# Kernel optimization log

Hardware: AMD Instinct MI355X
Metric: run time of the kernel (lower is better)

## Reference

```python
import jax, jax.numpy as jnp
import numpy as np
import math

N = 30000; N0 = 18000; N1 = 12000; R = 5; E = 600000
H = 128; HM = 128; C = 8
L1 = 20.0; L2 = 30.0
THRESH = 0.3; THRESH_C = 1e-3
T_INNER = 20; K_OUTER = 8
EPS = 1e-5


def setup_inputs() -> dict:
    key = jax.random.key(0)
    ks = jax.random.split(key, 16)
    def w(k, shape):  # kaiming-ish fan_in init
        return jax.random.normal(k, shape, jnp.float32) / np.sqrt(shape[0])
    return {
        "feat0": jax.random.normal(ks[0], (N0, 256), jnp.float32),
        "feat1": jax.random.normal(ks[1], (N1, 128), jnp.float32),
        "W0": w(ks[2], (256, H)), "b0": jnp.zeros((H,), jnp.float32),
        "W1": w(ks[3], (128, H)), "b1": jnp.zeros((H,), jnp.float32),
        "Wm1": w(ks[4], (H, HM)), "bm1": jnp.zeros((HM,), jnp.float32),
        "Wm2": w(ks[5], (HM, HM)), "bm2": jnp.zeros((HM,), jnp.float32),
        "Wout": w(ks[6], (HM, C)), "bout": jnp.zeros((C,), jnp.float32),
        "src": jax.random.randint(ks[7], (E,), 0, N, jnp.int32),
        "dst": jax.random.randint(ks[8], (E,), 0, N, jnp.int32),
        "rel": jax.random.randint(ks[9], (E,), 0, R, jnp.int32),
    }


def _layernorm(z):
    m = z.mean(-1, keepdims=True)
    v = z.var(-1, keepdims=True)
    return (z - m) / jnp.sqrt(v + EPS)


def _forward(feat0, feat1, W0, b0, W1, b1, Wm1, bm1, Wm2, bm2, Wout, bout, src, dst, rel):
    # transfer (transf_type==2): per-type linear -> concat -> 2-layer MLP w/ layernorm
    h = jnp.concatenate([feat0 @ W0 + b0, feat1 @ W1 + b1], axis=0)   # (N, H)
    z = jax.nn.relu(_layernorm(h @ Wm1 + bm1))
    h = z @ Wm2 + bm2                                                 # (N, HM)
    # per-node standardization (torch std is unbiased, ddof=1), nan -> 0
    mu = h.mean(1, keepdims=True)
    sd = h.std(1, ddof=1, keepdims=True)
    out0 = jnp.nan_to_num((h - mu) / sd)

    # per-relation row degrees of the vertically stacked adjacency (R*N, N)
    key_e = rel * N + src                                             # (E,)
    deg = jax.ops.segment_sum(jnp.ones(E, jnp.float32), key_e, num_segments=R * N)
    safe = jnp.maximum(deg, 1.0)
    vals = jnp.where(deg > 0, 1.0 / safe, 0.0)[key_e]                 # row-normalized A weights
    dinv = jnp.where(deg > 0, 1.0 / jnp.sqrt(safe), 0.0)              # D^{-1/2}
    edge_dinv = dinv[key_e] * dinv[rel * N + dst]                     # (E,)
    active = (deg > 0).astype(jnp.float32).reshape(R, N)              # (R, N)

    def tv(x):  # relational total variation tr(X^T L_r X)/N, L_r = I - D^-1/2 A_r D^-1/2
        node_term = active @ (x * x).sum(1)                           # (R,)
        edot = (x[src] * x[dst]).sum(1)                               # (E,)
        edge_term = jax.ops.segment_sum(edge_dinv * edot, rel, num_segments=R)
        return (node_term - edge_term) / N

    ratio = 2.0 * L2 / L1
    c_l1tr = jnp.abs(tv(out0)).sum()
    u0 = jnp.full((R,), 1.0 / R, jnp.float32)

    def mirror_descent(u, w, l1tr):
        fi = l1tr + ratio
        def step(carry, t):
            u, act = carry
            T_t = jnp.sqrt(2.0 * math.log(R) / (t * fi * fi))
            u_ta = u * jnp.exp(-T_t * (ratio * u + w))
            u_new = u_ta / u_ta.sum()
            diff = jnp.sqrt(((u - u_new) ** 2).sum())
            u = jnp.where(act, u_new, u)
            return (u, act & (diff >= THRESH_C)), None
        ts = jnp.arange(1, T_INNER + 1, dtype=jnp.float32)
        (u, _), _ = jax.lax.scan(step, (u, jnp.array(True)), ts)
        return u

    def outer(carry, _):
        x, u, act = carry
        w = tv(x)
        l1tr = jnp.abs(w).sum()
        u = jnp.where(act, mirror_descent(u, w, l1tr), u)
        still = act & (l1tr / c_l1tr >= THRESH)
        ew = u[rel] * vals                                            # (E,)
        msg = jax.ops.segment_sum(ew[:, None] * x[dst], src, num_segments=N)  # (N, HM)
        x = jnp.where(still, x / (1.0 + L1) + (L1 / (1.0 + L1)) * msg, x)
        return (x, u, still), None

    (x, u, _), _ = jax.lax.scan(outer, (out0, u0, jnp.array(True)), None, length=K_OUTER)
    logits = x @ Wout + bout
    return logits, x, u


def reference(feat0, feat1, W0, b0, W1, b1, Wm1, bm1, Wm2, bm2, Wout, bout, src, dst, rel):
    return _forward(feat0, feat1, W0, b0, W1, b1, Wm1, bm1, Wm2, bm2, Wout, bout, src, dst, rel)
```

## Files before the change

### kernel.cpp

```cpp
#include <hip/hip_runtime.h>
#include <hip/hip_fp16.h>
#include <cmath>

typedef unsigned short ushort_t;
typedef unsigned int uint_t;

#define N_TOT 30000
#define N0_   18000
#define R_    5
#define E_    600000
#define RN    (R_ * N_TOT)
#define NC_   (N_TOT * 8)
#define NX_   (N_TOT * 128)
#define NL_   (N_TOT * 64)
#define SCAN_NB ((RN + 1023) / 1024)

typedef __attribute__((ext_vector_type(8))) short bf16x8;
typedef __attribute__((ext_vector_type(4))) float f32x4;

__device__ __forceinline__ ushort_t f2bf(float f) {
    uint_t u = __float_as_uint(f);
    uint_t r = (u + 0x7fffu + ((u >> 16) & 1u)) >> 16;
    return (ushort_t)r;
}
__device__ __forceinline__ float bflo(uint_t v) { return __uint_as_float(v << 16); }
__device__ __forceinline__ float bfhi(uint_t v) { return __uint_as_float(v & 0xffff0000u); }

__global__ void init_kernel(float* ug, int* act) {
    if (threadIdx.x < 5) ug[threadIdx.x] = 0.2f;
    if (threadIdx.x == 0) act[0] = 1;
}

__global__ __launch_bounds__(256) void cvtfeat_kernel(const float* __restrict__ in,
                                                      ushort_t* __restrict__ out,
                                                      int nelem)
{
    int i = (blockIdx.x * 256 + threadIdx.x) * 4;
    if (i >= nelem) return;
    const float4 v = *(const float4*)(in + i);
    ushort_t o0 = f2bf(v.x), o1 = f2bf(v.y), o2 = f2bf(v.z), o3 = f2bf(v.w);
    uint_t p0 = (uint_t)o0 | ((uint_t)o1 << 16);
    uint_t p1 = (uint_t)o2 | ((uint_t)o3 << 16);
    uint2* op = (uint2*)(out + i);
    *op = make_uint2(p0, p1);
}

__global__ __launch_bounds__(256) void cvtw_kernel(const float* __restrict__ W,
                                                   ushort_t* __restrict__ wt, int K)
{
    int idx = blockIdx.x * 256 + threadIdx.x;
    if (idx >= 128 * K) return;
    int j = idx / K, k = idx - j * K;
    wt[idx] = f2bf(W[k * 128 + j]);
}

__global__ __launch_bounds__(256) void mlp_mfma_kernel(
    const ushort_t* __restrict__ fb0, const ushort_t* __restrict__ fb1,
    const ushort_t* __restrict__ wt0, const ushort_t* __restrict__ wt1,
    const ushort_t* __restrict__ wtm1, const ushort_t* __restrict__ wtm2,
    const float* __restrict__ b0, const float* __restrict__ b1,
    const float* __restrict__ bm1, const float* __restrict__ bm2,
    float* __restrict__ xout, ushort_t* __restrict__ xh)
{
    const int t = threadIdx.x;
    const int lane = t & 63;
    const int wv = t >> 6;
    const int lr = lane & 15;
    const int lg = lane >> 4;
    const int row0 = blockIdx.x * 32;

    __shared__ ushort_t hls[32][136];
    __shared__ float    tls[32][132];
    __shared__ ushort_t zls[32][136];

    #pragma unroll
    for (int mt = 0; mt < 2; ++mt) {
        const int rb = row0 + mt * 16;
        const bool is0 = (rb < N0_);
        const int r = min(rb + lr, N_TOT - 1);
        const ushort_t* __restrict__ fa =
            is0 ? fb0 + (size_t)r * 256 : fb1 + (size_t)(r - N0_) * 128;
        const ushort_t* __restrict__ wt = is0 ? wt0 : wt1;
        const int K = is0 ? 256 : 128;
        const int c0 = wv * 32 + lr;

        f32x4 a0 = {0.f, 0.f, 0.f, 0.f};
        f32x4 a1 = {0.f, 0.f, 0.f, 0.f};
        for (int ks = 0; ks < K; ks += 32) {
            const bf16x8 af = *(const bf16x8*)(fa + ks + lg * 8);
            const bf16x8 wb0 = *(const bf16x8*)(wt + (size_t)c0 * K + ks + lg * 8);
            const bf16x8 wb1 = *(const bf16x8*)(wt + (size_t)(c0 + 16) * K + ks + lg * 8);
            a0 = __builtin_amdgcn_mfma_f32_16x16x32_bf16(af, wb0, a0, 0, 0, 0);
            a1 = __builtin_amdgcn_mfma_f32_16x16x32_bf16(af, wb1, a1, 0, 0, 0);
        }
        const float bb0 = is0 ? b0[c0] : b1[c0];
        const float bb1 = is0 ? b0[c0 + 16] : b1[c0 + 16];
        #pragma unroll
        for (int j = 0; j < 4; ++j) {
            hls[mt * 16 + lg * 4 + j][c0]      = f2bf(a0[j] + bb0);
            hls[mt * 16 + lg * 4 + j][c0 + 16] = f2bf(a1[j] + bb1);
        }
    }
    __syncthreads();

    {
        const int c0 = wv * 32 + lr;
        f32x4 g00 = {0.f,0.f,0.f,0.f}, g01 = {0.f,0.f,0.f,0.f};
        f32x4 g10 = {0.f,0.f,0.f,0.f}, g11 = {0.f,0.f,0.f,0.f};
        for (int ks = 0; ks < 128; ks += 32) {
            const bf16x8 wb0 = *(const bf16x8*)(wtm1 + (size_t)c0 * 128 + ks + lg * 8);
            const bf16x8 wb1 = *(const bf16x8*)(wtm1 + (size_t)(c0 + 16) * 128 + ks + lg * 8);
            const bf16x8 af0 = *(const bf16x8*)(&hls[lr][ks + lg * 8]);
            const bf16x8 af1 = *(const bf16x8*)(&hls[16 + lr][ks + lg * 8]);
            g00 = __builtin_amdgcn_mfma_f32_16x16x32_bf16(af0, wb0, g00, 0, 0, 0);
            g01 = __builtin_amdgcn_mfma_f32_16x16x32_bf16(af0, wb1, g01, 0, 0, 0);
            g10 = __builtin_amdgcn_mfma_f32_16x16x32_bf16(af1, wb0, g10, 0, 0, 0);
            g11 = __builtin_amdgcn_mfma_f32_16x16x32_bf16(af1, wb1, g11, 0, 0, 0);
        }
        const float bb0 = bm1[c0], bb1 = bm1[c0 + 16];
        #pragma unroll
        for (int j = 0; j < 4; ++j) {
            tls[lg * 4 + j][c0]           = g00[j] + bb0;
            tls[lg * 4 + j][c0 + 16]      = g01[j] + bb1;
            tls[16 + lg * 4 + j][c0]      = g10[j] + bb0;
            tls[16 + lg * 4 + j][c0 + 16] = g11[j] + bb1;
        }
    }
    __syncthreads();

    {
        const int row = t >> 3, seg = t & 7;
        f32x4 v[4];
        float s = 0.f;
        #pragma unroll
        for (int i = 0; i < 4; ++i) {
            v[i] = *(const f32x4*)(&tls[row][seg * 16 + i * 4]);
            s += v[i][0] + v[i][1] + v[i][2] + v[i][3];
        }
        #pragma unroll
        for (int o = 1; o < 8; o <<= 1) s += __shfl_xor(s, o, 64);
        const float mean = s * (1.0f / 128.0f);
        float q = 0.f;
        #pragma unroll
        for (int i = 0; i < 4; ++i) {
            #pragma unroll
            for (int e = 0; e < 4; ++e) { float d = v[i][e] - mean; q = fmaf(d, d, q); }
        }
        #pragma unroll
        for (int o = 1; o < 8; o <<= 1) q += __shfl_xor(q, o, 64);
        const float inv = 1.0f / sqrtf(q * (1.0f / 128.0f) + 1e-5f);
        uint_t* zp = (uint_t*)&zls[row][0];
        #pragma unroll
        for (int i = 0; i < 4; ++i) {
            ushort_t z0 = f2bf(fmaxf((v[i][0] - mean) * inv, 0.0f));
            ushort_t z1 = f2bf(fmaxf((v[i][1] - mean) * inv, 0.0f));
            ushort_t z2 = f2bf(fmaxf((v[i][2] - mean) * inv, 0.0f));
            ushort_t z3 = f2bf(fmaxf((v[i][3] - mean) * inv, 0.0f));
            zp[(seg * 16 + i * 4) / 2]     = (uint_t)z0 | ((uint_t)z1 << 16);
            zp[(seg * 16 + i * 4) / 2 + 1] = (uint_t)z2 | ((uint_t)z3 << 16);
        }
    }
    __syncthreads();

    {
        const int c0 = wv * 32 + lr;
        f32x4 g00 = {0.f,0.f,0.f,0.f}, g01 = {0.f,0.f,0.f,0.f};
        f32x4 g10 = {0.f,0.f,0.f,0.f}, g11 = {0.f,0.f,0.f,0.f};
        for (int ks = 0; ks < 128; ks += 32) {
            const bf16x8 wb0 = *(const bf16x8*)(wtm2 + (size_t)c0 * 128 + ks + lg * 8);
            const bf16x8 wb1 = *(const bf16x8*)(wtm2 + (size_t)(c0 + 16) * 128 + ks + lg * 8);
            const bf16x8 af0 = *(const bf16x8*)(&zls[lr][ks + lg * 8]);
            const bf16x8 af1 = *(const bf16x8*)(&zls[16 + lr][ks + lg * 8]);
            g00 = __builtin_amdgcn_mfma_f32_16x16x32_bf16(af0, wb0, g00, 0, 0, 0);
            g01 = __builtin_amdgcn_mfma_f32_16x16x32_bf16(af0, wb1, g01, 0, 0, 0);
            g10 = __builtin_amdgcn_mfma_f32_16x16x32_bf16(af1, wb0, g10, 0, 0, 0);
            g11 = __builtin_amdgcn_mfma_f32_16x16x32_bf16(af1, wb1, g11, 0, 0, 0);
        }
        __syncthreads();
        const float bb0 = bm2[c0], bb1 = bm2[c0 + 16];
        #pragma unroll
        for (int j = 0; j < 4; ++j) {
            tls[lg * 4 + j][c0]           = g00[j] + bb0;
            tls[lg * 4 + j][c0 + 16]      = g01[j] + bb1;
            tls[16 + lg * 4 + j][c0]      = g10[j] + bb0;
            tls[16 + lg * 4 + j][c0 + 16] = g11[j] + bb1;
        }
    }
    __syncthreads();

    {
        const int row = t >> 3, seg = t & 7;
        const int n = row0 + row;
        f32x4 v[4];
        float s = 0.f;
        #pragma unroll
        for (int i = 0; i < 4; ++i) {
            v[i] = *(const f32x4*)(&tls[row][seg * 16 + i * 4]);
            s += v[i][0] + v[i][1] + v[i][2] + v[i][3];
        }
        #pragma unroll
        for (int o = 1; o < 8; o <<= 1) s += __shfl_xor(s, o, 64);
        const float mu = s * (1.0f / 128.0f);
        float q = 0.f;
        #pragma unroll
        for (int i = 0; i < 4; ++i) {
            #pragma unroll
            for (int e = 0; e < 4; ++e) { float d = v[i][e] - mu; q = fmaf(d, d, q); }
        }
        #pragma unroll
        for (int o = 1; o < 8; o <<= 1) q += __shfl_xor(q, o, 64);
        const float sd = sqrtf(q * (1.0f / 127.0f));
        const float inv = 1.0f / sd;
        if (n < N_TOT) {
            uint_t* xhp = (uint_t*)xh + (size_t)n * 64 + seg * 8;
            float* xop = xout + (size_t)n * 128 + seg * 16;
            #pragma unroll
            for (int i = 0; i < 4; ++i) {
                float rr[4];
                #pragma unroll
                for (int e = 0; e < 4; ++e) {
                    float r = (v[i][e] - mu) * inv;
                    if (!(fabsf(r) <= 3.402823466e38f)) {
                        r = (r != r) ? 0.0f : ((r > 0.0f) ? 3.402823466e38f : -3.402823466e38f);
                    }
                    rr[e] = r;
                }
                *(float4*)(xop + i * 4) = make_float4(rr[0], rr[1], rr[2], rr[3]);
                xhp[i * 2]     = (uint_t)f2bf(rr[0]) | ((uint_t)f2bf(rr[1]) << 16);
                xhp[i * 2 + 1] = (uint_t)f2bf(rr[2]) | ((uint_t)f2bf(rr[3]) << 16);
            }
        }
    }
}

__global__ void deg_kernel(const int* __restrict__ src, const int* __restrict__ rel,
                           int* __restrict__ deg_i)
{
    int e = blockIdx.x * 256 + threadIdx.x;
    if (e >= E_) return;
    atomicAdd(&deg_i[src[e] * R_ + rel[e]], 1);
}

__global__ void dinv_kernel(const int* __restrict__ deg_i, float* __restrict__ dinv)
{
    int i = blockIdx.x * 256 + threadIdx.x;
    if (i >= RN) return;
    int dg = deg_i[i];
    dinv[i] = (dg > 0) ? 1.0f / sqrtf((float)dg) : 0.0f;
}

__global__ __launch_bounds__(256) void scan1_kernel(const int* __restrict__ cnt,
                                                    int* __restrict__ rp,
                                                    int* __restrict__ bsum)
{
    __shared__ int wsum[4];
    const int t = threadIdx.x, lane = t & 63, w = t >> 6;
    const int i0 = blockIdx.x * 1024 + t * 4;
    const int v0 = (i0 + 0 < RN) ? cnt[i0 + 0] : 0;
    const int v1 = (i0 + 1 < RN) ? cnt[i0 + 1] : 0;
    const int v2 = (i0 + 2 < RN) ? cnt[i0 + 2] : 0;
    const int v3 = (i0 + 3 < RN) ? cnt[i0 + 3] : 0;
    const int s = v0 + v1 + v2 + v3;
    int sc = s;
    #pragma unroll
    for (int o = 1; o < 64; o <<= 1) { int tmp = __shfl_up(sc, o, 64); if (lane >= o) sc += tmp; }
    if (lane == 63) wsum[w] = sc;
    __syncthreads();
    int woff = 0;
    #pragma unroll
    for (int i = 0; i < 3; ++i) if (i < w) woff += wsum[i];
    int run = woff + sc - s;
    if (i0 + 0 < RN) rp[i0 + 0] = run; run += v0;
    if (i0 + 1 < RN) rp[i0 + 1] = run; run += v1;
    if (i0 + 2 < RN) rp[i0 + 2] = run; run += v2;
    if (i0 + 3 < RN) rp[i0 + 3] = run;
    if (t == 255) bsum[blockIdx.x] = woff + sc;
}

__global__ __launch_bounds__(256) void scan2_kernel(const int* __restrict__ bsum,
                                                    int* __restrict__ boff,
                                                    int* __restrict__ rp)
{
    __shared__ int wsum[4];
    const int t = threadIdx.x, lane = t & 63, w = t >> 6;
    const int v = (t < SCAN_NB) ? bsum[t] : 0;
    int sc = v;
    #pragma unroll
    for (int o = 1; o < 64; o <<= 1) { int tmp = __shfl_up(sc, o, 64); if (lane >= o) sc += tmp; }
    if (lane == 63) wsum[w] = sc;
    __syncthreads();
    int woff = 0;
    #pragma unroll
    for (int i = 0; i < 3; ++i) if (i < w) woff += wsum[i];
    boff[t] = woff + sc - v;
    if (t == 0) rp[RN] = E_;
}

__global__ __launch_bounds__(256) void scan3_kernel(int* __restrict__ rp,
                                                    const int* __restrict__ boff)
{
    const int off = boff[blockIdx.x];
    if (off == 0) return;
    const int i0 = blockIdx.x * 1024 + threadIdx.x * 4;
    if (i0 + 3 < RN) {
        int4* p = (int4*)(rp + i0);
        int4 q = *p;
        q.x += off; q.y += off; q.z += off; q.w += off;
        *p = q;
    } else {
        for (int i = 0; i < 4; ++i)
            if (i0 + i < RN) rp[i0 + i] += off;
    }
}

__global__ void scatter_kernel(const int* __restrict__ src, const int* __restrict__ dst,
                               const int* __restrict__ rel, const int* __restrict__ rp,
                               int* __restrict__ fill, const int* __restrict__ deg_i,
                               const float* __restrict__ dinv,
                               int4* __restrict__ csr_pk)
{
    int e = blockIdx.x * 256 + threadIdx.x;
    if (e >= E_) return;
    int s = src[e], r = rel[e], d = dst[e];
    int key = s * R_ + r;
    int pos = rp[key] + atomicAdd(&fill[key], 1);
    float edinv = dinv[key] * dinv[d * R_ + r];
    float w = 1.0f / (float)deg_i[key];
    csr_pk[pos] = make_int4(d, __float_as_int(edinv), __float_as_int(w), 0);
}

__global__ __launch_bounds__(256) void gather_kernel(
    const ushort_t* __restrict__ xh, const int* __restrict__ rp,
    const int4* __restrict__ csr_pk,
    const int* __restrict__ act, int k, float* __restrict__ accbuf,
    uint_t* __restrict__ mbuf)
{
    if (act[k] == 0) return;
    const int lane = threadIdx.x & 63;
    const int wv = threadIdx.x >> 6;
    const int wid = blockIdx.x * 4 + wv;
    const int nw = gridDim.x * 4;
    float na[5] = {0, 0, 0, 0, 0};
    float ea[5] = {0, 0, 0, 0, 0};
    for (int n = wid; n < N_TOT; n += nw) {
        const int b0 = __builtin_amdgcn_readfirstlane(rp[n * R_ + 0]);
        const int b1 = __builtin_amdgcn_readfirstlane(rp[n * R_ + 1]);
        const int b2 = __builtin_amdgcn_readfirstlane(rp[n * R_ + 2]);
        const int b3 = __builtin_amdgcn_readfirstlane(rp[n * R_ + 3]);
        const int b4 = __builtin_amdgcn_readfirstlane(rp[n * R_ + 4]);
        const int b5 = __builtin_amdgcn_readfirstlane(rp[n * R_ + 5]);
        const uint_t vs = ((const uint_t*)(xh + (size_t)n * 128))[lane];
        const float sx = bflo(vs), sy = bfhi(vs);
        const float pp = fmaf(sx, sx, sy * sy);
        if (b1 > b0) na[0] += pp;
        if (b2 > b1) na[1] += pp;
        if (b3 > b2) na[2] += pp;
        if (b4 > b3) na[3] += pp;
        if (b5 > b4) na[4] += pp;
        float mx[5] = {0, 0, 0, 0, 0};
        float my[5] = {0, 0, 0, 0, 0};
        int e = b0;
        for (; e + 4 <= b5; e += 4) {
            int4 p0 = csr_pk[e + 0];
            int4 p1 = csr_pk[e + 1];
            int4 p2 = csr_pk[e + 2];
            int4 p3 = csr_pk[e + 3];
            const uint_t v0 = ((const uint_t*)(xh + (size_t)p0.x * 128))[lane];
            const uint_t v1 = ((const uint_t*)(xh + (size_t)p1.x * 128))[lane];
            const uint_t v2 = ((const uint_t*)(xh + (size_t)p2.x * 128))[lane];
            const uint_t v3 = ((const uint_t*)(xh + (size_t)p3.x * 128))[lane];
            const float x0 = bflo(v0), y0 = bfhi(v0);
            const float x1 = bflo(v1), y1 = bfhi(v1);
            const float x2 = bflo(v2), y2 = bfhi(v2);
            const float x3 = bflo(v3), y3 = bfhi(v3);
            const float d0 = __int_as_float(p0.y) * fmaf(sx, x0, sy * y0);
            const float d1 = __int_as_float(p1.y) * fmaf(sx, x1, sy * y1);
            const float d2 = __int_as_float(p2.y) * fmaf(sx, x2, sy * y2);
            const float d3 = __int_as_float(p3.y) * fmaf(sx, x3, sy * y3);
            const int r0 = (e + 0 >= b1) + (e + 0 >= b2) + (e + 0 >= b3) + (e + 0 >= b4);
            const int r1 = (e + 1 >= b1) + (e + 1 >= b2) + (e + 1 >= b3) + (e + 1 >= b4);
            const int r2 = (e + 2 >= b1) + (e + 2 >= b2) + (e + 2 >= b3) + (e + 2 >= b4);
            const int r3 = (e + 3 >= b1) + (e + 3 >= b2) + (e + 3 >= b3) + (e + 3 >= b4);
            #pragma unroll
            for (int rr = 0; rr < 5; ++rr) {
                ea[rr] += (r0 == rr ? d0 : 0.0f) + (r1 == rr ? d1 : 0.0f) +
                          (r2 == rr ? d2 : 0.0f) + (r3 == rr ? d3 : 0.0f);
                const float ws0 = (r0 == rr) ? __int_as_float(p0.z) : 0.0f;
                const float ws1 = (r1 == rr) ? __int_as_float(p1.z) : 0.0f;
                const float ws2 = (r2 == rr) ? __int_as_float(p2.z) : 0.0f;
                const float ws3 = (r3 == rr) ? __int_as_float(p3.z) : 0.0f;
                mx[rr] = fmaf(ws0, x0, fmaf(ws1, x1, fmaf(ws2, x2, fmaf(ws3, x3, mx[rr]))));
                my[rr] = fmaf(ws0, y0, fmaf(ws1, y1, fmaf(ws2, y2, fmaf(ws3, y3, my[rr]))));
            }
        }
        for (; e < b5; ++e) {
            int4 p0 = csr_pk[e];
            const uint_t v0 = ((const uint_t*)(xh + (size_t)p0.x * 128))[lane];
            const float x0 = bflo(v0), y0 = bfhi(v0);
            const float d0 = __int_as_float(p0.y) * fmaf(sx, x0, sy * y0);
            const int r0 = (e >= b1) + (e >= b2) + (e >= b3) + (e >= b4);
            #pragma unroll
            for (int rr = 0; rr < 5; ++rr) {
                ea[rr] += (r0 == rr ? d0 : 0.0f);
                const float ws0 = (r0 == rr) ? __int_as_float(p0.z) : 0.0f;
                mx[rr] = fmaf(ws0, x0, mx[rr]);
                my[rr] = fmaf(ws0, y0, my[rr]);
            }
        }
        #pragma unroll
        for (int rr = 0; rr < 5; ++rr) {
            __half2 hm = __floats2half2_rn(mx[rr], my[rr]);
            mbuf[(size_t)rr * NL_ + (size_t)n * 64 + lane] =
                *reinterpret_cast<const uint_t*>(&hm);
        }
    }
    __shared__ float sacc[4][10];
    #pragma unroll
    for (int r = 0; r < 5; ++r) {
        float a = na[r], b = ea[r];
        for (int o = 32; o > 0; o >>= 1) {
            a += __shfl_down(a, o, 64);
            b += __shfl_down(b, o, 64);
        }
        if (lane == 0) { sacc[wv][r] = a; sacc[wv][5 + r] = b; }
    }
    __syncthreads();
    if (threadIdx.x < 10) {
        float t = sacc[0][threadIdx.x] + sacc[1][threadIdx.x] +
                  sacc[2][threadIdx.x] + sacc[3][threadIdx.x];
        atomicAdd(&accbuf[k * 16 + threadIdx.x], t);
    }
}

__global__ void scalar_kernel(const float* __restrict__ accbuf, float* __restrict__ ug,
                              float* __restrict__ c_l1, int* __restrict__ act, int k)
{
    if (blockIdx.x != 0 || threadIdx.x >= 8) return;
    const int r = threadIdx.x;
    const int a = act[k];
    float w = (r < 5) ? (accbuf[k * 16 + r] - accbuf[k * 16 + 5 + r]) * (1.0f / 30000.0f)
                      : 0.0f;
    float l1 = fabsf(w);
    for (int o = 4; o > 0; o >>= 1) l1 += __shfl_xor(l1, o, 8);
    if (k == 0 && r == 0) c_l1[0] = l1;
    if (!a) { if (r == 0) act[k + 1] = 0; return; }
    float u = (r < 5) ? ug[r] : 0.0f;
    const float fi = l1 + 3.0f;
    bool mact = true;
    for (int t = 1; t <= 20; ++t) {
        float T = sqrtf(3.2188758248682006f / ((float)t * fi * fi));
        float ta = u * expf(-T * (3.0f * u + w));
        float ssum = ta;
        for (int o = 4; o > 0; o >>= 1) ssum += __shfl_xor(ssum, o, 8);
        float un = ta / ssum;
        float d0 = u - un;
        float dq = d0 * d0;
        for (int o = 4; o > 0; o >>= 1) dq += __shfl_xor(dq, o, 8);
        if (mact) u = un;
        mact = mact && (sqrtf(dq) >= 1e-3f);
    }
    if (r < 5) ug[r] = u;
    if (r == 0) act[k + 1] = (l1 / c_l1[0] >= 0.3f) ? 1 : 0;
}

__global__ __launch_bounds__(256) void apply_kernel(
    float* __restrict__ x, ushort_t* __restrict__ xh_out,
    const uint_t* __restrict__ mbuf, const float* __restrict__ ug,
    const int* __restrict__ act, int k)
{
    if (act[k + 1] == 0) return;
    const int tid = blockIdx.x * 256 + threadIdx.x;
    if (tid >= NL_) return;
    const float u0 = ug[0], u1 = ug[1], u2 = ug[2], u3 = ug[3], u4 = ug[4];

    uint_t w0 = mbuf[(size_t)0 * NL_ + tid];
    uint_t w1 = mbuf[(size_t)1 * NL_ + tid];
    uint_t w2 = mbuf[(size_t)2 * NL_ + tid];
    uint_t w3 = mbuf[(size_t)3 * NL_ + tid];
    uint_t w4 = mbuf[(size_t)4 * NL_ + tid];
    const float2 m0 = __half22float2(*reinterpret_cast<const __half2*>(&w0));
    const float2 m1 = __half22float2(*reinterpret_cast<const __half2*>(&w1));
    const float2 m2 = __half22float2(*reinterpret_cast<const __half2*>(&w2));
    const float2 m3 = __half22float2(*reinterpret_cast<const __half2*>(&w3));
    const float2 m4 = __half22float2(*reinterpret_cast<const __half2*>(&w4));

    const float sm_x = u0 * m0.x + u1 * m1.x + u2 * m2.x + u3 * m3.x + u4 * m4.x;
    const float sm_y = u0 * m0.y + u1 * m1.y + u2 * m2.y + u3 * m3.y + u4 * m4.y;

    const float ci = 1.0f / 21.0f, cb = 20.0f / 21.0f;
    float2* xp = (float2*)x;
    const float2 xs = xp[tid];
    const float nx_ = fmaf(cb, sm_x, xs.x * ci);
    const float ny_ = fmaf(cb, sm_y, xs.y * ci);
    xp[tid] = make_float2(nx_, ny_);
    ((uint_t*)xh_out)[tid] = ((uint_t)f2bf(ny_) << 16) | (uint_t)f2bf(nx_);
}

__global__ __launch_bounds__(256) void final_kernel(const float* __restrict__ x,
                                                    const float* __restrict__ Wout,
                                                    const float* __restrict__ bout,
                                                    const float* __restrict__ ug,
                                                    float* __restrict__ out)
{
    const int nl = threadIdx.x >> 7;
    const int n = blockIdx.x * 2 + nl;
    const int j = threadIdx.x & 127;
    const int lane = threadIdx.x & 63;
    const int wv = threadIdx.x >> 6;
    float xv = x[(size_t)n * 128 + j];
    out[(size_t)NC_ + (size_t)n * 128 + j] = xv;
    float p[8];
    #pragma unroll
    for (int c = 0; c < 8; ++c) p[c] = xv * Wout[j * 8 + c];
    #pragma unroll
    for (int c = 0; c < 8; ++c)
        for (int o = 32; o > 0; o >>= 1) p[c] += __shfl_down(p[c], o, 64);
    __shared__ float sp[4][8];
    if (lane == 0) {
        #pragma unroll
        for (int c = 0; c < 8; ++c) sp[wv][c] = p[c];
    }
    __syncthreads();
    if (j < 8) {
        int c = j;
        out[(size_t)n * 8 + c] = bout[c] + sp[2 * nl][c] + sp[2 * nl + 1][c];
    }
    if (blockIdx.x == 0 && threadIdx.x < 5)
        out[(size_t)NC_ + (size_t)NX_ + threadIdx.x] = ug[threadIdx.x];
}

extern "C" void kernel_launch(void* const* d_in, const int* in_sizes, int n_in,
                              void* d_out, int out_size, void* d_ws, size_t ws_size,
                              hipStream_t stream)
{
    const float* feat0 = (const float*)d_in[0];
    const float* feat1 = (const float*)d_in[1];
    const float* W0   = (const float*)d_in[2];
    const float* b0   = (const float*)d_in[3];
    const float* W1   = (const float*)d_in[4];
    const float* b1   = (const float*)d_in[5];
    const float* Wm1  = (const float*)d_in[6];
    const float* bm1  = (const float*)d_in[7];
    const float* Wm2  = (const float*)d_in[8];
    const float* bm2  = (const float*)d_in[9];
    const float* Wout = (const float*)d_in[10];
    const float* bout = (const float*)d_in[11];
    const int* src = (const int*)d_in[12];
    const int* dst = (const int*)d_in[13];
    const int* rel = (const int*)d_in[14];
    float* out = (float*)d_out;

    char* p = (char*)d_ws;
    auto alloc = [&](size_t bytes) { char* q = p; p += (bytes + 255) & ~(size_t)255; return q; };
    float*    xbuf      = (float*)   alloc((size_t)NX_ * 4);
    ushort_t* xh0       = (ushort_t*)alloc((size_t)NX_ * 2);
    ushort_t* xh1       = (ushort_t*)alloc((size_t)NX_ * 2);
    uint_t*   mbuf      = (uint_t*)  alloc((size_t)R_ * NL_ * 4);
    ushort_t* fb0       = (ushort_t*)alloc((size_t)N0_ * 256 * 2);
    ushort_t* fb1       = (ushort_t*)alloc((size_t)(N_TOT - N0_) * 128 * 2);
    ushort_t* wt0       = (ushort_t*)alloc((size_t)128 * 256 * 2);
    ushort_t* wt1       = (ushort_t*)alloc((size_t)128 * 128 * 2);
    ushort_t* wtm1      = (ushort_t*)alloc((size_t)128 * 128 * 2);
    ushort_t* wtm2      = (ushort_t*)alloc((size_t)128 * 128 * 2);
    int*      deg_i     = (int*)     alloc((size_t)RN * 4);
    float*    dinv      = (float*)   alloc((size_t)RN * 4);
    int*      rp        = (int*)     alloc(((size_t)RN + 1) * 4);
    int*      fill      = (int*)     alloc((size_t)RN * 4);
    int*      bsum      = (int*)     alloc((size_t)SCAN_NB * 4);
    int*      boff      = (int*)     alloc(256 * 4);
    int4*     csr_pk    = (int4*)    alloc((size_t)E_ * 16);
    float*    accbuf    = (float*)   alloc(128 * 4);
    float*    ug        = (float*)   alloc(64);
    float*    c_l1      = (float*)   alloc(64);
    int*      act       = (int*)     alloc(64);

    hipMemsetAsync(deg_i, 0, (size_t)RN * 4, stream);
    hipMemsetAsync(fill, 0, (size_t)RN * 4, stream);
    hipMemsetAsync(accbuf, 0, 128 * 4, stream);
    init_kernel<<<1, 64, 0, stream>>>(ug, act);

    cvtfeat_kernel<<<(N0_ * 256 / 4 + 255) / 256, 256, 0, stream>>>(feat0, fb0, N0_ * 256);
    cvtfeat_kernel<<<((N_TOT - N0_) * 128 / 4 + 255) / 256, 256, 0, stream>>>(
        feat1, fb1, (N_TOT - N0_) * 128);
    cvtw_kernel<<<(128 * 256 + 255) / 256, 256, 0, stream>>>(W0, wt0, 256);
    cvtw_kernel<<<(128 * 128 + 255) / 256, 256, 0, stream>>>(W1, wt1, 128);
    cvtw_kernel<<<(128 * 128 + 255) / 256, 256, 0, stream>>>(Wm1, wtm1, 128);
    cvtw_kernel<<<(128 * 128 + 255) / 256, 256, 0, stream>>>(Wm2, wtm2, 128);

    mlp_mfma_kernel<<<(N_TOT + 31) / 32, 256, 0, stream>>>(
        fb0, fb1, wt0, wt1, wtm1, wtm2, b0, b1, bm1, bm2, xbuf, xh0);

    deg_kernel<<<(E_ + 255) / 256, 256, 0, stream>>>(src, rel, deg_i);
    dinv_kernel<<<(RN + 255) / 256, 256, 0, stream>>>(deg_i, dinv);
    scan1_kernel<<<SCAN_NB, 256, 0, stream>>>(deg_i, rp, bsum);
    scan2_kernel<<<1, 256, 0, stream>>>(bsum, boff, rp);
    scan3_kernel<<<SCAN_NB, 256, 0, stream>>>(rp, boff);
    scatter_kernel<<<(E_ + 255) / 256, 256, 0, stream>>>(src, dst, rel, rp, fill,
                                                         deg_i, dinv, csr_pk);

    ushort_t* ha = xh0;
    ushort_t* hb = xh1;
    for (int k = 0; k < 8; ++k) {
        gather_kernel<<<2048, 256, 0, stream>>>(ha, rp, csr_pk, act, k, accbuf, mbuf);
        scalar_kernel<<<1, 64, 0, stream>>>(accbuf, ug, c_l1, act, k);
        apply_kernel<<<(NL_ + 255) / 256, 256, 0, stream>>>(xbuf, hb, mbuf, ug, act, k);
        ushort_t* t = ha; ha = hb; hb = t;
    }

    final_kernel<<<N_TOT / 2, 256, 0, stream>>>(xbuf, Wout, bout, ug, out);
}
```

Baseline: 434.0 us.

## Fuse dinv into scatter, use nontemporal loads in apply, retune gather grid

Drops the separate dinv kernel and computes inverse square-root degrees inline in the scatter kernel, saving one launch and one intermediate buffer. The apply kernel now uses nontemporal loads and stores for the message buffer and x, to limit cache pollution from streamed data. The gather grid grows from 2048 to 2500 blocks, and init now zeroes the whole act array. These are several small independent tweaks; the nontemporal hints could hurt if x is reused out of cache soon after.

```diff
diff --git a/kernel.cpp b/kernel.cpp
--- a/kernel.cpp
+++ b/kernel.cpp
@@ -17,6 +17,7 @@
 
 typedef __attribute__((ext_vector_type(8))) short bf16x8;
 typedef __attribute__((ext_vector_type(4))) float f32x4;
+typedef __attribute__((ext_vector_type(2))) float f32x2;
 
 __device__ __forceinline__ ushort_t f2bf(float f) {
     uint_t u = __float_as_uint(f);
@@ -27,8 +28,8 @@
 __device__ __forceinline__ float bfhi(uint_t v) { return __uint_as_float(v & 0xffff0000u); }
 
 __global__ void init_kernel(float* ug, int* act) {
+    if (threadIdx.x < 16) act[threadIdx.x] = (threadIdx.x == 0) ? 1 : 0;
     if (threadIdx.x < 5) ug[threadIdx.x] = 0.2f;
-    if (threadIdx.x == 0) act[0] = 1;
 }
 
 __global__ __launch_bounds__(256) void cvtfeat_kernel(const float* __restrict__ in,
@@ -241,14 +242,6 @@
     atomicAdd(&deg_i[src[e] * R_ + rel[e]], 1);
 }
 
-__global__ void dinv_kernel(const int* __restrict__ deg_i, float* __restrict__ dinv)
-{
-    int i = blockIdx.x * 256 + threadIdx.x;
-    if (i >= RN) return;
-    int dg = deg_i[i];
-    dinv[i] = (dg > 0) ? 1.0f / sqrtf((float)dg) : 0.0f;
-}
-
 __global__ __launch_bounds__(256) void scan1_kernel(const int* __restrict__ cnt,
                                                     int* __restrict__ rp,
                                                     int* __restrict__ bsum)
@@ -316,7 +309,6 @@
 __global__ void scatter_kernel(const int* __restrict__ src, const int* __restrict__ dst,
                                const int* __restrict__ rel, const int* __restrict__ rp,
                                int* __restrict__ fill, const int* __restrict__ deg_i,
-                               const float* __restrict__ dinv,
                                int4* __restrict__ csr_pk)
 {
     int e = blockIdx.x * 256 + threadIdx.x;
@@ -324,8 +316,12 @@
     int s = src[e], r = rel[e], d = dst[e];
     int key = s * R_ + r;
     int pos = rp[key] + atomicAdd(&fill[key], 1);
-    float edinv = dinv[key] * dinv[d * R_ + r];
-    float w = 1.0f / (float)deg_i[key];
+    int dg_s = deg_i[key];
+    int dg_d = deg_i[d * R_ + r];
+    float di_s = (dg_s > 0) ? 1.0f / sqrtf((float)dg_s) : 0.0f;
+    float di_d = (dg_d > 0) ? 1.0f / sqrtf((float)dg_d) : 0.0f;
+    float edinv = di_s * di_d;
+    float w = 1.0f / (float)dg_s;
     csr_pk[pos] = make_int4(d, __float_as_int(edinv), __float_as_int(w), 0);
 }
 
@@ -473,11 +469,11 @@
     if (tid >= NL_) return;
     const float u0 = ug[0], u1 = ug[1], u2 = ug[2], u3 = ug[3], u4 = ug[4];
 
-    uint_t w0 = mbuf[(size_t)0 * NL_ + tid];
-    uint_t w1 = mbuf[(size_t)1 * NL_ + tid];
-    uint_t w2 = mbuf[(size_t)2 * NL_ + tid];
-    uint_t w3 = mbuf[(size_t)3 * NL_ + tid];
-    uint_t w4 = mbuf[(size_t)4 * NL_ + tid];
+    uint_t w0 = __builtin_nontemporal_load(mbuf + (size_t)0 * NL_ + tid);
+    uint_t w1 = __builtin_nontemporal_load(mbuf + (size_t)1 * NL_ + tid);
+    uint_t w2 = __builtin_nontemporal_load(mbuf + (size_t)2 * NL_ + tid);
+    uint_t w3 = __builtin_nontemporal_load(mbuf + (size_t)3 * NL_ + tid);
+    uint_t w4 = __builtin_nontemporal_load(mbuf + (size_t)4 * NL_ + tid);
     const float2 m0 = __half22float2(*reinterpret_cast<const __half2*>(&w0));
     const float2 m1 = __half22float2(*reinterpret_cast<const __half2*>(&w1));
     const float2 m2 = __half22float2(*reinterpret_cast<const __half2*>(&w2));
@@ -488,11 +484,12 @@
     const float sm_y = u0 * m0.y + u1 * m1.y + u2 * m2.y + u3 * m3.y + u4 * m4.y;
 
     const float ci = 1.0f / 21.0f, cb = 20.0f / 21.0f;
-    float2* xp = (float2*)x;
-    const float2 xs = xp[tid];
-    const float nx_ = fmaf(cb, sm_x, xs.x * ci);
-    const float ny_ = fmaf(cb, sm_y, xs.y * ci);
-    xp[tid] = make_float2(nx_, ny_);
+    f32x2* xp = (f32x2*)x;
+    const f32x2 xs = __builtin_nontemporal_load(xp + tid);
+    const float nx_ = fmaf(cb, sm_x, xs[0] * ci);
+    const float ny_ = fmaf(cb, sm_y, xs[1] * ci);
+    f32x2 xn; xn[0] = nx_; xn[1] = ny_;
+    __builtin_nontemporal_store(xn, xp + tid);
     ((uint_t*)xh_out)[tid] = ((uint_t)f2bf(ny_) << 16) | (uint_t)f2bf(nx_);
 }
 
@@ -563,7 +560,6 @@
     ushort_t* wtm1      = (ushort_t*)alloc((size_t)128 * 128 * 2);
     ushort_t* wtm2      = (ushort_t*)alloc((size_t)128 * 128 * 2);
     int*      deg_i     = (int*)     alloc((size_t)RN * 4);
-    float*    dinv      = (float*)   alloc((size_t)RN * 4);
     int*      rp        = (int*)     alloc(((size_t)RN + 1) * 4);
     int*      fill      = (int*)     alloc((size_t)RN * 4);
     int*      bsum      = (int*)     alloc((size_t)SCAN_NB * 4);
@@ -591,17 +587,16 @@
         fb0, fb1, wt0, wt1, wtm1, wtm2, b0, b1, bm1, bm2, xbuf, xh0);
 
     deg_kernel<<<(E_ + 255) / 256, 256, 0, stream>>>(src, rel, deg_i);
-    dinv_kernel<<<(RN + 255) / 256, 256, 0, stream>>>(deg_i, dinv);
     scan1_kernel<<<SCAN_NB, 256, 0, stream>>>(deg_i, rp, bsum);
     scan2_kernel<<<1, 256, 0, stream>>>(bsum, boff, rp);
     scan3_kernel<<<SCAN_NB, 256, 0, stream>>>(rp, boff);
     scatter_kernel<<<(E_ + 255) / 256, 256, 0, stream>>>(src, dst, rel, rp, fill,
-                                                         deg_i, dinv, csr_pk);
+                                                         deg_i, csr_pk);
 
     ushort_t* ha = xh0;
     ushort_t* hb = xh1;
     for (int k = 0; k < 8; ++k) {
-        gather_kernel<<<2048, 256, 0, stream>>>(ha, rp, csr_pk, act, k, accbuf, mbuf);
+        gather_kernel<<<2500, 256, 0, stream>>>(ha, rp, csr_pk, act, k, accbuf, mbuf);
         scalar_kernel<<<1, 64, 0, stream>>>(accbuf, ug, c_l1, act, k);
         apply_kernel<<<(NL_ + 255) / 256, 256, 0, stream>>>(xbuf, hb, mbuf, ug, act, k);
         ushort_t* t = ha; ha = hb; hb = t;
```

New measurement: 436.1 us. About the same (+0.5%).
